# Kernel tuning notes

Measured on AMD Instinct MI355X. Metric: run time of the kernel, lower is better.

Reference implementation:

```python
import jax, jax.numpy as jnp
import numpy as np

B, S, D = 2, 2048, 1024
H = 16
HD = D // H  # head_dim = 64
NEG = -1e30  # finite stand-in for -inf; masked entries are zeroed after softmax so math matches


def setup_inputs() -> dict:
    key = jax.random.key(0)
    ks = jax.random.split(key, 10)
    q = jax.random.normal(ks[0], (B, S, D), dtype=jnp.float32)
    k = jax.random.normal(ks[1], (B, S, D), dtype=jnp.float32)
    v = jax.random.normal(ks[2], (B, S, D), dtype=jnp.float32)
    mask = jax.random.randint(ks[3], (B, S), 0, 2).astype(bool)
    s = 1.0 / np.sqrt(D)
    Wq = jax.random.uniform(ks[4], (D, D), jnp.float32, -s, s)
    bq = jax.random.uniform(ks[5], (D,), jnp.float32, -s, s)
    Wk = jax.random.uniform(ks[6], (D, D), jnp.float32, -s, s)
    bk = jax.random.uniform(ks[7], (D,), jnp.float32, -s, s)
    Wv = jax.random.uniform(ks[8], (D, D), jnp.float32, -s, s)
    bv = jax.random.uniform(ks[9], (D,), jnp.float32, -s, s)
    return {"q": q, "k": k, "v": v, "mask": mask,
            "Wq": Wq, "bq": bq, "Wk": Wk, "bk": bk, "Wv": Wv, "bv": bv}


def _split_heads(x):
    # [B,S,D] -> [H,B,S,HD]  (matches permute(2,0,1,3) in torch)
    return x.reshape(B, S, H, HD).transpose(2, 0, 1, 3)


def reference(q, k, v, mask, Wq, bq, Wk, bk, Wv, bv):
    mq = _split_heads(q @ Wq.T + bq)
    mk = _split_heads(k @ Wk.T + bk)
    mv = _split_heads(v @ Wv.T + bv)
    # scores: [H,B,Sq,Sk]
    scores = jnp.einsum('hbqd,hbkd->hbqk', mq, mk) / jnp.sqrt(jnp.float32(HD))
    pair_mask = (mask[:, :, None] & mask[:, None, :])[None]  # [1,B,S,S]
    scores = jnp.where(pair_mask, scores, NEG)
    attn = jax.nn.softmax(scores, axis=-1)
    attn = jnp.where(pair_mask, attn, 0.0)
    out = jnp.einsum('hbqk,hbkd->hbqd', attn, mv)
    # [H,B,S,HD] -> [B,S,D]
    return out.transpose(1, 2, 0, 3).reshape(B, S, H * HD)
```

## Files before the change

kernel.cpp:

```cpp
#include <hip/hip_runtime.h>
#include <math.h>

#define B_ 2
#define S_ 2048
#define D_ 1024
#define H_ 16
#define HD_ 64

#define LOG2E 1.44269504088896f

typedef __bf16 bf16_t;
typedef bf16_t bf16x8 __attribute__((ext_vector_type(8)));
typedef bf16_t bf16x4v __attribute__((ext_vector_type(4)));
typedef float f32x4 __attribute__((ext_vector_type(4)));

#define GLOBAL_LOAD_LDS16(gp, lp)                                              \
    __builtin_amdgcn_global_load_lds(                                          \
        (const __attribute__((address_space(1))) void*)(gp),                   \
        (__attribute__((address_space(3))) void*)(lp), 16, 0, 0)

__global__ __launch_bounds__(256) void cvt_kernel(
    const float* __restrict__ q, const float* __restrict__ k,
    const float* __restrict__ v, const float* __restrict__ wq,
    const float* __restrict__ wk, const float* __restrict__ wv,
    const int* __restrict__ msk,
    bf16_t* __restrict__ qb, bf16_t* __restrict__ kb, bf16_t* __restrict__ vb,
    bf16_t* __restrict__ wqb, bf16_t* __restrict__ wkb, bf16_t* __restrict__ wvb,
    float* __restrict__ kbias)
{
    const int y = blockIdx.y;
    size_t idx = ((size_t)blockIdx.x * 256 + threadIdx.x) * 4;

    if (y == 6) {
        if (idx >= (size_t)B_ * S_) return;
        int4 mi = *(const int4*)(msk + idx);
        const float vb_ = -8.0f * LOG2E;
        float4 o4;
        o4.x = mi.x ? vb_ : -1e30f;
        o4.y = mi.y ? vb_ : -1e30f;
        o4.z = mi.z ? vb_ : -1e30f;
        o4.w = mi.w ? vb_ : -1e30f;
        *(float4*)(kbias + idx) = o4;
        return;
    }

    const float* src;
    bf16_t* dst;
    size_t n;
    switch (y) {
        case 0: src = q;  dst = qb;  n = (size_t)B_ * S_ * D_; break;
        case 1: src = k;  dst = kb;  n = (size_t)B_ * S_ * D_; break;
        case 2: src = v;  dst = vb;  n = (size_t)B_ * S_ * D_; break;
        case 3: src = wq; dst = wqb; n = (size_t)D_ * D_;      break;
        case 4: src = wk; dst = wkb; n = (size_t)D_ * D_;      break;
        default: src = wv; dst = wvb; n = (size_t)D_ * D_;     break;
    }
    if (idx >= n) return;
    float4 f = *(const float4*)(src + idx);
    bf16x4v o;
    o[0] = (bf16_t)f.x; o[1] = (bf16_t)f.y;
    o[2] = (bf16_t)f.z; o[3] = (bf16_t)f.w;
    *(bf16x4v*)(dst + idx) = o;
}

__global__ __launch_bounds__(256) void proj_mfma(
    const bf16_t* __restrict__ X0, const bf16_t* __restrict__ X1,
    const bf16_t* __restrict__ X2, const bf16_t* __restrict__ W0,
    const bf16_t* __restrict__ W1, const bf16_t* __restrict__ W2,
    const float* __restrict__ b0, const float* __restrict__ b1,
    const float* __restrict__ b2, bf16_t* __restrict__ o0,
    bf16_t* __restrict__ o1, bf16_t* __restrict__ o2)
{
    __shared__ __align__(16) bf16_t As[128 * 32];
    __shared__ __align__(16) bf16_t Bs[128 * 32];

    const int z = blockIdx.z;
    const bf16_t* X = (z == 0) ? X0 : (z == 1) ? X1 : X2;
    const bf16_t* W = (z == 0) ? W0 : (z == 1) ? W1 : W2;
    const float* bias = (z == 0) ? b0 : (z == 1) ? b1 : b2;
    bf16_t* out = (z == 0) ? o0 : (z == 1) ? o1 : o2;
    const float oscale = (z == 0) ? 0.125f * LOG2E : 1.0f;

    const int tid  = threadIdx.x;
    const int w    = tid >> 6;
    const int lane = tid & 63;
    const int L    = lane & 15;
    const int quad = lane >> 4;
    const int wr   = (w >> 1) * 64;
    const int wc   = (w & 1) * 64;
    const int row0 = blockIdx.x * 128;
    const int col0 = blockIdx.y * 128;

    const int lr = lane >> 2;
    const int lc = (lane & 3) * 8;

    f32x4 acc[4][4];
    #pragma unroll
    for (int i = 0; i < 4; ++i)
        #pragma unroll
        for (int j = 0; j < 4; ++j) {
            acc[i][j][0] = 0.f; acc[i][j][1] = 0.f;
            acc[i][j][2] = 0.f; acc[i][j][3] = 0.f;
        }

    for (int k0 = 0; k0 < D_; k0 += 32) {
        __syncthreads();
        #pragma unroll
        for (int i = 0; i < 2; ++i) {
            const int rA = i * 64 + w * 16;
            GLOBAL_LOAD_LDS16(X + (size_t)(row0 + rA + lr) * D_ + k0 + lc,
                              &As[rA * 32]);
            GLOBAL_LOAD_LDS16(W + (size_t)(col0 + rA + lr) * D_ + k0 + lc,
                              &Bs[rA * 32]);
        }
        __syncthreads();

        bf16x8 aF[4], bF[4];
        #pragma unroll
        for (int t = 0; t < 4; ++t) {
            aF[t] = *(const bf16x8*)&As[(wr + t * 16 + L) * 32 + quad * 8];
            bF[t] = *(const bf16x8*)&Bs[(wc + t * 16 + L) * 32 + quad * 8];
        }
        #pragma unroll
        for (int mt = 0; mt < 4; ++mt)
            #pragma unroll
            for (int nt = 0; nt < 4; ++nt)
                acc[mt][nt] = __builtin_amdgcn_mfma_f32_16x16x32_bf16(
                    aF[mt], bF[nt], acc[mt][nt], 0, 0, 0);
    }

    if (z == 2) {
        #pragma unroll
        for (int nt = 0; nt < 4; ++nt) {
            const int j  = col0 + wc + nt * 16 + L;
            const float bval = bias[j];
            const int h  = j >> 6;
            const int hd = j & 63;
            #pragma unroll
            for (int mt = 0; mt < 4; ++mt) {
                const int n = row0 + wr + mt * 16 + quad * 4;
                const int b = n >> 11;
                const int s = n & (S_ - 1);
                bf16x4v r4;
                #pragma unroll
                for (int r = 0; r < 4; ++r)
                    r4[r] = (bf16_t)(acc[mt][nt][r] + bval);
                *(bf16x4v*)(out + (((size_t)b * H_ + h) * HD_ + hd) * S_ + s) = r4;
            }
        }
    } else {
        #pragma unroll
        for (int nt = 0; nt < 4; ++nt) {
            const int j  = col0 + wc + nt * 16 + L;
            const float bval = bias[j];
            const int h  = j >> 6;
            const int hd = j & 63;
            #pragma unroll
            for (int mt = 0; mt < 4; ++mt)
                #pragma unroll
                for (int r = 0; r < 4; ++r) {
                    const int n = row0 + wr + mt * 16 + quad * 4 + r;
                    const int b = n >> 11;
                    const int s = n & (S_ - 1);
                    out[((((size_t)b * H_ + h) * S_ + s) * HD_) + hd] =
                        (bf16_t)((acc[mt][nt][r] + bval) * oscale);
                }
        }
    }
}

__global__ __launch_bounds__(256) void attn_kernel(
    const bf16_t* __restrict__ Q, const bf16_t* __restrict__ K,
    const bf16_t* __restrict__ Vt, const float* __restrict__ kbias,
    const int* __restrict__ mask, float* __restrict__ out)
{
    constexpr int LD = 72;
    __shared__ bf16_t Ks[64 * LD];
    __shared__ bf16_t Vs[64 * LD];
    __shared__ bf16_t Pt[4][32 * LD];

    const int tid  = threadIdx.x;
    const int w    = tid >> 6;
    const int lane = tid & 63;
    const int L    = lane & 15;
    const int quad = lane >> 4;
    const int h    = blockIdx.y;
    const int b    = blockIdx.z;
    const int bh   = b * H_ + h;
    const int q0   = blockIdx.x * 128;

    const bf16_t* kbase = K  + (size_t)bh * S_ * HD_;
    const bf16_t* vbase = Vt + (size_t)bh * HD_ * S_;
    const float*  bbase = kbias + b * S_;
    const int*    mrow  = mask + b * S_;

    const int sr  = tid >> 3;
    const int sc2 = (tid & 7) * 8;

    bf16x8 aQ[2][2];
    #pragma unroll
    for (int qb = 0; qb < 2; ++qb) {
        const bf16_t* qp = Q + ((size_t)bh * S_ + q0 + w * 32 + qb * 16 + L) * HD_;
        aQ[qb][0] = *(const bf16x8*)(qp + quad * 8);
        aQ[qb][1] = *(const bf16x8*)(qp + 32 + quad * 8);
    }

    f32x4 o[2][4];
    #pragma unroll
    for (int qb = 0; qb < 2; ++qb)
        #pragma unroll
        for (int f = 0; f < 4; ++f) {
            o[qb][f][0]=0.f; o[qb][f][1]=0.f; o[qb][f][2]=0.f; o[qb][f][3]=0.f;
        }
    float l_[2] = {0.f, 0.f};

    bf16x8 kr0, kr1, vr0, vr1;
    f32x4  bias_n[4];
    {
        kr0 = *(const bf16x8*)(kbase + (size_t)sr * HD_ + sc2);
        kr1 = *(const bf16x8*)(kbase + (size_t)(sr + 32) * HD_ + sc2);
        vr0 = *(const bf16x8*)(vbase + (size_t)sr * S_ + sc2);
        vr1 = *(const bf16x8*)(vbase + (size_t)(sr + 32) * S_ + sc2);
        #pragma unroll
        for (int f = 0; f < 4; ++f)
            bias_n[f] = *(const f32x4*)(bbase + f * 16 + quad * 4);
    }

    for (int kt = 0; kt < S_; kt += 64) {
        __syncthreads();
        *(bf16x8*)&Ks[sr * LD + sc2]        = kr0;
        *(bf16x8*)&Ks[(sr + 32) * LD + sc2] = kr1;
        *(bf16x8*)&Vs[sr * LD + sc2]        = vr0;
        *(bf16x8*)&Vs[(sr + 32) * LD + sc2] = vr1;
        f32x4 bias_c[4];
        #pragma unroll
        for (int f = 0; f < 4; ++f) bias_c[f] = bias_n[f];
        __syncthreads();

        if (kt + 64 < S_) {
            const int kn = kt + 64;
            kr0 = *(const bf16x8*)(kbase + (size_t)(kn + sr) * HD_ + sc2);
            kr1 = *(const bf16x8*)(kbase + (size_t)(kn + sr + 32) * HD_ + sc2);
            vr0 = *(const bf16x8*)(vbase + (size_t)sr * S_ + kn + sc2);
            vr1 = *(const bf16x8*)(vbase + (size_t)(sr + 32) * S_ + kn + sc2);
            #pragma unroll
            for (int f = 0; f < 4; ++f)
                bias_n[f] = *(const f32x4*)(bbase + kn + f * 16 + quad * 4);
        }

        bf16x8 aK[4][2];
        #pragma unroll
        for (int f = 0; f < 4; ++f) {
            aK[f][0] = *(const bf16x8*)&Ks[(f * 16 + L) * LD + quad * 8];
            aK[f][1] = *(const bf16x8*)&Ks[(f * 16 + L) * LD + 32 + quad * 8];
        }

        bf16_t* pw = &Pt[w][0];
        #pragma unroll
        for (int qb = 0; qb < 2; ++qb) {
            #pragma unroll
            for (int f = 0; f < 4; ++f) {
                f32x4 z = bias_c[f];
                z = __builtin_amdgcn_mfma_f32_16x16x32_bf16(aK[f][0], aQ[qb][0], z, 0, 0, 0);
                z = __builtin_amdgcn_mfma_f32_16x16x32_bf16(aK[f][1], aQ[qb][1], z, 0, 0, 0);
                float e0 = exp2f(z[0]);
                float e1 = exp2f(z[1]);
                float e2 = exp2f(z[2]);
                float e3 = exp2f(z[3]);
                l_[qb] += (e0 + e1) + (e2 + e3);
                bf16x4v p4;
                p4[0] = (bf16_t)e0; p4[1] = (bf16_t)e1;
                p4[2] = (bf16_t)e2; p4[3] = (bf16_t)e3;
                *(bf16x4v*)&pw[(qb * 16 + L) * LD + f * 16 + quad * 4] = p4;
            }
        }

        bf16x8 aP[2][2];
        #pragma unroll
        for (int qb = 0; qb < 2; ++qb) {
            aP[qb][0] = *(const bf16x8*)&pw[(qb * 16 + L) * LD + quad * 8];
            aP[qb][1] = *(const bf16x8*)&pw[(qb * 16 + L) * LD + 32 + quad * 8];
        }

        #pragma unroll
        for (int f = 0; f < 4; ++f) {
            bf16x8 bV0 = *(const bf16x8*)&Vs[(f * 16 + L) * LD + quad * 8];
            bf16x8 bV1 = *(const bf16x8*)&Vs[(f * 16 + L) * LD + 32 + quad * 8];
            #pragma unroll
            for (int qb = 0; qb < 2; ++qb) {
                o[qb][f] = __builtin_amdgcn_mfma_f32_16x16x32_bf16(aP[qb][0], bV0, o[qb][f], 0, 0, 0);
                o[qb][f] = __builtin_amdgcn_mfma_f32_16x16x32_bf16(aP[qb][1], bV1, o[qb][f], 0, 0, 0);
            }
        }
    }

    #pragma unroll
    for (int qb = 0; qb < 2; ++qb) {
        float t = l_[qb];
        t += __shfl_xor(t, 16);
        t += __shfl_xor(t, 32);
        int qv = mrow[q0 + w * 32 + qb * 16 + L];
        l_[qb] = (qv && t > 0.f) ? (1.0f / t) : 0.0f;
    }

    #pragma unroll
    for (int qb = 0; qb < 2; ++qb) {
        float inv[4];
        #pragma unroll
        for (int r = 0; r < 4; ++r)
            inv[r] = __shfl(l_[qb], quad * 4 + r);
        float* obase = out + ((size_t)b * S_ + q0 + w * 32 + qb * 16 + quad * 4) * D_ + h * HD_;
        #pragma unroll
        for (int f = 0; f < 4; ++f)
            #pragma unroll
            for (int r = 0; r < 4; ++r)
                obase[r * D_ + f * 16 + L] = o[qb][f][r] * inv[r];
    }
}

extern "C" void kernel_launch(void* const* d_in, const int* in_sizes, int n_in,
                              void* d_out, int out_size, void* d_ws, size_t ws_size,
                              hipStream_t stream)
{
    const float* q    = (const float*)d_in[0];
    const float* k    = (const float*)d_in[1];
    const float* v    = (const float*)d_in[2];
    const int*   mask = (const int*)d_in[3];
    const float* Wq   = (const float*)d_in[4];
    const float* bq   = (const float*)d_in[5];
    const float* Wk   = (const float*)d_in[6];
    const float* bk   = (const float*)d_in[7];
    const float* Wv   = (const float*)d_in[8];
    const float* bv   = (const float*)d_in[9];
    float* out = (float*)d_out;

    const size_t PE = (size_t)B_ * S_ * D_;
    const size_t WE = (size_t)D_ * D_;

    bf16_t* qb    = (bf16_t*)d_ws;
    bf16_t* kb    = qb + PE;
    bf16_t* vb    = kb + PE;
    bf16_t* wqb   = vb + PE;
    bf16_t* wkb   = wqb + WE;
    bf16_t* wvb   = wkb + WE;
    bf16_t* mq    = wvb + WE;
    bf16_t* mk    = mq + PE;
    bf16_t* vt    = mk + PE;
    float*  kbias = (float*)(vt + PE);

    dim3 cgrid(PE / (256 * 4), 7);
    cvt_kernel<<<cgrid, 256, 0, stream>>>(q, k, v, Wq, Wk, Wv, mask,
                                          qb, kb, vb, wqb, wkb, wvb, kbias);

    dim3 pgrid(4096 / 128, 1024 / 128, 3);
    proj_mfma<<<pgrid, 256, 0, stream>>>(qb, kb, vb, wqb, wkb, wvb,
                                         bq, bk, bv, mq, mk, vt);

    dim3 agrid(S_ / 128, H_, B_);
    attn_kernel<<<agrid, 256, 0, stream>>>(mq, mk, vt, kbias, mask, out);
}
```

Before: 227.7 us.

## Compact convert grid, transpose Q/K projection for vector stores, use raw exp2

The convert kernel now uses a flat 1D grid sized to the real work instead of a 7-row grid in which most blocks for the weights and mask exit immediately. The Q/K projection swaps its operands so that each lane holds four consecutive head-dim values, which lets the epilogue write bf16x4 vectors instead of scalar bf16 stores. The softmax exponential uses the hardware exp2 builtin in place of exp2f, which removes range handling. These are three separate small changes spread across all three kernels.

```diff
diff --git a/kernel.cpp b/kernel.cpp
--- a/kernel.cpp
+++ b/kernel.cpp
@@ -8,11 +8,22 @@
 #define HD_ 64
 
 #define LOG2E 1.44269504088896f
+#define LN2   0.69314718055994531f
 
 typedef __bf16 bf16_t;
 typedef bf16_t bf16x8 __attribute__((ext_vector_type(8)));
 typedef bf16_t bf16x4v __attribute__((ext_vector_type(4)));
 typedef float f32x4 __attribute__((ext_vector_type(4)));
+
+#if defined(__has_builtin)
+#  if __has_builtin(__builtin_amdgcn_exp2f)
+#    define EXP2(x) __builtin_amdgcn_exp2f(x)
+#  else
+#    define EXP2(x) __expf((x) * LN2)
+#  endif
+#else
+#  define EXP2(x) __expf((x) * LN2)
+#endif
 
 #define GLOBAL_LOAD_LDS16(gp, lp)                                              \
     __builtin_amdgcn_global_load_lds(                                          \
@@ -28,11 +39,23 @@
     bf16_t* __restrict__ wqb, bf16_t* __restrict__ wkb, bf16_t* __restrict__ wvb,
     float* __restrict__ kbias)
 {
-    const int y = blockIdx.y;
-    size_t idx = ((size_t)blockIdx.x * 256 + threadIdx.x) * 4;
-
-    if (y == 6) {
-        if (idx >= (size_t)B_ * S_) return;
+    const int bid = blockIdx.x;
+    const float* src;
+    bf16_t* dst;
+    int x;
+
+    if (bid < 12288) {
+        int y = bid >> 12;
+        x = bid & 4095;
+        src = (y == 0) ? q : (y == 1) ? k : v;
+        dst = (y == 0) ? qb : (y == 1) ? kb : vb;
+    } else if (bid < 15360) {
+        int y = (bid - 12288) >> 10;
+        x = (bid - 12288) & 1023;
+        src = (y == 0) ? wq : (y == 1) ? wk : wv;
+        dst = (y == 0) ? wqb : (y == 1) ? wkb : wvb;
+    } else {
+        size_t idx = ((size_t)(bid - 15360) * 256 + threadIdx.x) * 4;
         int4 mi = *(const int4*)(msk + idx);
         const float vb_ = -8.0f * LOG2E;
         float4 o4;
@@ -44,18 +67,7 @@
         return;
     }
 
-    const float* src;
-    bf16_t* dst;
-    size_t n;
-    switch (y) {
-        case 0: src = q;  dst = qb;  n = (size_t)B_ * S_ * D_; break;
-        case 1: src = k;  dst = kb;  n = (size_t)B_ * S_ * D_; break;
-        case 2: src = v;  dst = vb;  n = (size_t)B_ * S_ * D_; break;
-        case 3: src = wq; dst = wqb; n = (size_t)D_ * D_;      break;
-        case 4: src = wk; dst = wkb; n = (size_t)D_ * D_;      break;
-        default: src = wv; dst = wvb; n = (size_t)D_ * D_;     break;
-    }
-    if (idx >= n) return;
+    size_t idx = ((size_t)x * 256 + threadIdx.x) * 4;
     float4 f = *(const float4*)(src + idx);
     bf16x4v o;
     o[0] = (bf16_t)f.x; o[1] = (bf16_t)f.y;
@@ -79,7 +91,11 @@
     const bf16_t* W = (z == 0) ? W0 : (z == 1) ? W1 : W2;
     const float* bias = (z == 0) ? b0 : (z == 1) ? b1 : b2;
     bf16_t* out = (z == 0) ? o0 : (z == 1) ? o1 : o2;
-    const float oscale = (z == 0) ? 0.125f * LOG2E : 1.0f;
+
+    const bf16_t* Amat = (z == 2) ? X : W;
+    const bf16_t* Bmat = (z == 2) ? W : X;
+    const int arow0 = (z == 2) ? blockIdx.x * 128 : blockIdx.y * 128;
+    const int brow0 = (z == 2) ? blockIdx.y * 128 : blockIdx.x * 128;
 
     const int tid  = threadIdx.x;
     const int w    = tid >> 6;
@@ -88,8 +104,6 @@
     const int quad = lane >> 4;
     const int wr   = (w >> 1) * 64;
     const int wc   = (w & 1) * 64;
-    const int row0 = blockIdx.x * 128;
-    const int col0 = blockIdx.y * 128;
 
     const int lr = lane >> 2;
     const int lc = (lane & 3) * 8;
@@ -108,9 +122,9 @@
         #pragma unroll
         for (int i = 0; i < 2; ++i) {
             const int rA = i * 64 + w * 16;
-            GLOBAL_LOAD_LDS16(X + (size_t)(row0 + rA + lr) * D_ + k0 + lc,
+            GLOBAL_LOAD_LDS16(Amat + (size_t)(arow0 + rA + lr) * D_ + k0 + lc,
                               &As[rA * 32]);
-            GLOBAL_LOAD_LDS16(W + (size_t)(col0 + rA + lr) * D_ + k0 + lc,
+            GLOBAL_LOAD_LDS16(Bmat + (size_t)(brow0 + rA + lr) * D_ + k0 + lc,
                               &Bs[rA * 32]);
         }
         __syncthreads();
@@ -132,13 +146,13 @@
     if (z == 2) {
         #pragma unroll
         for (int nt = 0; nt < 4; ++nt) {
-            const int j  = col0 + wc + nt * 16 + L;
+            const int j  = brow0 + wc + nt * 16 + L;
             const float bval = bias[j];
             const int h  = j >> 6;
             const int hd = j & 63;
             #pragma unroll
             for (int mt = 0; mt < 4; ++mt) {
-                const int n = row0 + wr + mt * 16 + quad * 4;
+                const int n = arow0 + wr + mt * 16 + quad * 4;
                 const int b = n >> 11;
                 const int s = n & (S_ - 1);
                 bf16x4v r4;
@@ -149,22 +163,24 @@
             }
         }
     } else {
-        #pragma unroll
-        for (int nt = 0; nt < 4; ++nt) {
-            const int j  = col0 + wc + nt * 16 + L;
-            const float bval = bias[j];
-            const int h  = j >> 6;
-            const int hd = j & 63;
-            #pragma unroll
-            for (int mt = 0; mt < 4; ++mt)
+        const float oscale = (z == 0) ? 0.125f * LOG2E : 1.0f;
+        #pragma unroll
+        for (int mt = 0; mt < 4; ++mt) {
+            const int j4 = arow0 + wr + mt * 16 + quad * 4;
+            const int h  = j4 >> 6;
+            const int hd = j4 & 63;
+            const f32x4 b4 = *(const f32x4*)(bias + j4);
+            #pragma unroll
+            for (int nt = 0; nt < 4; ++nt) {
+                const int n = brow0 + wc + nt * 16 + L;
+                const int b = n >> 11;
+                const int s = n & (S_ - 1);
+                bf16x4v r4;
                 #pragma unroll
-                for (int r = 0; r < 4; ++r) {
-                    const int n = row0 + wr + mt * 16 + quad * 4 + r;
-                    const int b = n >> 11;
-                    const int s = n & (S_ - 1);
-                    out[((((size_t)b * H_ + h) * S_ + s) * HD_) + hd] =
-                        (bf16_t)((acc[mt][nt][r] + bval) * oscale);
-                }
+                for (int r = 0; r < 4; ++r)
+                    r4[r] = (bf16_t)((acc[mt][nt][r] + b4[r]) * oscale);
+                *(bf16x4v*)(out + ((((size_t)b * H_ + h) * S_ + s) * HD_) + hd) = r4;
+            }
         }
     }
 }
@@ -263,10 +279,10 @@
                 f32x4 z = bias_c[f];
                 z = __builtin_amdgcn_mfma_f32_16x16x32_bf16(aK[f][0], aQ[qb][0], z, 0, 0, 0);
                 z = __builtin_amdgcn_mfma_f32_16x16x32_bf16(aK[f][1], aQ[qb][1], z, 0, 0, 0);
-                float e0 = exp2f(z[0]);
-                float e1 = exp2f(z[1]);
-                float e2 = exp2f(z[2]);
-                float e3 = exp2f(z[3]);
+                float e0 = EXP2(z[0]);
+                float e1 = EXP2(z[1]);
+                float e2 = EXP2(z[2]);
+                float e3 = EXP2(z[3]);
                 l_[qb] += (e0 + e1) + (e2 + e3);
                 bf16x4v p4;
                 p4[0] = (bf16_t)e0; p4[1] = (bf16_t)e1;
@@ -348,9 +364,8 @@
     bf16_t* vt    = mk + PE;
     float*  kbias = (float*)(vt + PE);
 
-    dim3 cgrid(PE / (256 * 4), 7);
-    cvt_kernel<<<cgrid, 256, 0, stream>>>(q, k, v, Wq, Wk, Wv, mask,
-                                          qb, kb, vb, wqb, wkb, wvb, kbias);
+    cvt_kernel<<<dim3(15364), 256, 0, stream>>>(q, k, v, Wq, Wk, Wv, mask,
+                                                qb, kb, vb, wqb, wkb, wvb, kbias);
 
     dim3 pgrid(4096 / 128, 1024 / 128, 3);
     proj_mfma<<<pgrid, 256, 0, stream>>>(qb, kb, vb, wqb, wkb, wvb,
```

New measurement: 212.5 us. 1.07x faster.
